# Kernel tuning notes

Hardware: AMD Instinct MI355X
Metric: run time of the kernel (lower is better)

## Reference

```python
import jax, jax.numpy as jnp
import numpy as np

BITS = 8
STEP = 2.0 ** (-5)
QMIN = -2.0 ** (BITS - 1)
QMAX = 2.0 ** (BITS - 1) - 1


def _q(x):
    # DFXP fixed-point fake-quantize: clamp(round(x/step), qmin, qmax)*step
    return jnp.clip(jnp.round(x / STEP), QMIN, QMAX) * STEP


@jax.custom_vjp
def fq(x):
    # ForwardQuantizer: quantize in fwd, straight-through grad
    return _q(x)

def _fq_fwd(x):
    return _q(x), None

def _fq_bwd(_, g):
    return (g,)

fq.defvjp(_fq_fwd, _fq_bwd)


def gq(x):
    # BackwardQuantizer: identity in forward (grad quantized only in bwd pass)
    return x


def setup_inputs() -> dict:
    key = jax.random.key(0)
    ks = jax.random.split(key, 5)
    B, I, H = 2048, 1024, 1024
    return {
        "X": jax.random.normal(ks[0], (B, I), dtype=jnp.float32),
        "h": jax.random.normal(ks[1], (B, H), dtype=jnp.float32),
        "c": jax.random.normal(ks[2], (B, H), dtype=jnp.float32),
        "weight": jax.random.normal(ks[3], (4 * H, I + H), dtype=jnp.float32) * (H ** -0.5),
        "bias": jax.random.normal(ks[4], (4 * H,), dtype=jnp.float32) * (H ** -0.5),
    }


def reference(X, h, c, weight, bias):
    # concat + input/weight/bias fake-quant
    Xh = fq(jnp.concatenate([X, h], axis=1))          # [B, I+H]
    Wq = fq(weight)                                    # [4H, I+H]
    bq = fq(bias)                                      # [4H]
    y = gq(Xh @ Wq.T + bq)                             # [B, 4H]
    i, f, g, o = jnp.split(y, 4, axis=1)
    i = fq(gq(jax.nn.sigmoid(i)))
    f = fq(gq(jax.nn.sigmoid(f)))
    g = fq(gq(jnp.tanh(g)))
    o = fq(gq(jax.nn.sigmoid(o)))
    cq = fq(c)
    c_new = gq(cq * f) + gq(i * g)
    cell_tanh = fq(gq(jnp.tanh(c_new)))
    h_new = gq(cell_tanh * o)
    return (h_new, c_new)
```

## Files before the change

### kernel.cpp

```cpp
#include <hip/hip_runtime.h>
#include <stdint.h>

#define B_DIM 2048
#define K_DIM 2048
#define N_PACK 4096

typedef int v4i __attribute__((ext_vector_type(4)));

__device__ __forceinline__ float fqf(float x) {
    float q = rintf(x * 32.0f);
    q = fminf(fmaxf(q, -128.0f), 127.0f);
    return q * 0.03125f;
}
__device__ __forceinline__ int q8i(float x) {
    float q = rintf(x * 32.0f);
    q = fminf(fmaxf(q, -128.0f), 127.0f);
    return (int)q;
}
__device__ __forceinline__ float fsigm(float x) {
    return __fdividef(1.0f, 1.0f + __expf(-x));
}
__device__ __forceinline__ float ftanh(float x) {
    return __fdividef(2.0f, 1.0f + __expf(-2.0f * x)) - 1.0f;
}

__global__ __launch_bounds__(256) void quant_pack(
    const float* __restrict__ X, const float* __restrict__ hI,
    const float* __restrict__ W, const float* __restrict__ bias,
    int8_t* __restrict__ Xhq, int8_t* __restrict__ Wq, float* __restrict__ bqp)
{
    const int bid = blockIdx.x;
    const int t = threadIdx.x;
    if (bid < 1024) {
        const int m = bid * 2 + (t >> 7);
        const int k0 = (t & 127) * 16;
        const float* src = (k0 < 1024) ? (X + (size_t)m * 1024 + k0)
                                       : (hI + (size_t)m * 1024 + (k0 - 1024));
        float4 v0 = *(const float4*)src;
        float4 v1 = *(const float4*)(src + 4);
        float4 v2 = *(const float4*)(src + 8);
        float4 v3 = *(const float4*)(src + 12);
        union { int8_t c[16]; v4i q; } u;
        u.c[0]  = (int8_t)q8i(v0.x); u.c[1]  = (int8_t)q8i(v0.y);
        u.c[2]  = (int8_t)q8i(v0.z); u.c[3]  = (int8_t)q8i(v0.w);
        u.c[4]  = (int8_t)q8i(v1.x); u.c[5]  = (int8_t)q8i(v1.y);
        u.c[6]  = (int8_t)q8i(v1.z); u.c[7]  = (int8_t)q8i(v1.w);
        u.c[8]  = (int8_t)q8i(v2.x); u.c[9]  = (int8_t)q8i(v2.y);
        u.c[10] = (int8_t)q8i(v2.z); u.c[11] = (int8_t)q8i(v2.w);
        u.c[12] = (int8_t)q8i(v3.x); u.c[13] = (int8_t)q8i(v3.y);
        u.c[14] = (int8_t)q8i(v3.z); u.c[15] = (int8_t)q8i(v3.w);
        *(v4i*)(Xhq + (size_t)m * K_DIM + k0) = u.q;
    } else if (bid < 3072) {
        const int r = (bid - 1024) * 2 + (t >> 7);
        const int gate = r >> 10, j = r & 1023;
        const int p = (j << 2) | gate;
        const int k0 = (t & 127) * 16;
        const float* src = W + (size_t)r * K_DIM + k0;
        float4 v0 = *(const float4*)src;
        float4 v1 = *(const float4*)(src + 4);
        float4 v2 = *(const float4*)(src + 8);
        float4 v3 = *(const float4*)(src + 12);
        union { int8_t c[16]; v4i q; } u;
        u.c[0]  = (int8_t)q8i(v0.x); u.c[1]  = (int8_t)q8i(v0.y);
        u.c[2]  = (int8_t)q8i(v0.z); u.c[3]  = (int8_t)q8i(v0.w);
        u.c[4]  = (int8_t)q8i(v1.x); u.c[5]  = (int8_t)q8i(v1.y);
        u.c[6]  = (int8_t)q8i(v1.z); u.c[7]  = (int8_t)q8i(v1.w);
        u.c[8]  = (int8_t)q8i(v2.x); u.c[9]  = (int8_t)q8i(v2.y);
        u.c[10] = (int8_t)q8i(v2.z); u.c[11] = (int8_t)q8i(v2.w);
        u.c[12] = (int8_t)q8i(v3.x); u.c[13] = (int8_t)q8i(v3.y);
        u.c[14] = (int8_t)q8i(v3.z); u.c[15] = (int8_t)q8i(v3.w);
        *(v4i*)(Wq + (size_t)p * K_DIM + k0) = u.q;
    } else {
        for (int idx = t; idx < N_PACK; idx += 256) {
            const int gate = idx >> 10, j = idx & 1023;
            bqp[(j << 2) | gate] = fqf(bias[idx]);
        }
    }
}

__global__ __launch_bounds__(512) void lstm_gemm(
    const int8_t* __restrict__ Xhq, const int8_t* __restrict__ Wq,
    const float* __restrict__ bqp, const float* __restrict__ cin,
    float* __restrict__ hout, float* __restrict__ cout_)
{
    __shared__ __align__(16) char raw[65536];
    const int t = threadIdx.x;
    const int l = t & 63;
    const int wave = t >> 6;
    const int wm = wave >> 2;
    const int wn = wave & 3;

    const int b = blockIdx.x;
    const int xcd = b & 7;
    const int slot = b >> 3;
    const int mt = ((xcd & 1) << 3) + (slot & 7);
    const int nt = ((xcd >> 1) << 3) + (slot >> 3);
    const int m0 = mt * 128;
    const int n0 = nt * 128;

    v4i acc[4][2];
    #pragma unroll
    for (int i = 0; i < 4; ++i)
        #pragma unroll
        for (int j = 0; j < 2; ++j)
            acc[i][j] = (v4i)0;

    const int srow = t >> 3;
    const int schunk = (t & 7) ^ (srow & 7);
    const int8_t* gA = Xhq + (size_t)(m0 + srow) * K_DIM + schunk * 16;
    const int8_t* gB = Wq  + (size_t)(n0 + srow) * K_DIM + schunk * 16;

    const int rrow = l & 15;
    const int lx = l & 7;

#define STAGE(p, kt) do { \
    char* Ad_ = raw + (p) * 32768; \
    char* Bd_ = raw + (p) * 32768 + 16384; \
    _Pragma("unroll") \
    for (int i_ = 0; i_ < 2; ++i_) { \
        __builtin_amdgcn_global_load_lds( \
            (const __attribute__((address_space(1))) uint32_t*)(gA + (size_t)(i_ * 64) * K_DIM + (kt) * 128), \
            (__attribute__((address_space(3))) uint32_t*)(Ad_ + i_ * 8192 + t * 16), 16, 0, 0); \
        __builtin_amdgcn_global_load_lds( \
            (const __attribute__((address_space(1))) uint32_t*)(gB + (size_t)(i_ * 64) * K_DIM + (kt) * 128), \
            (__attribute__((address_space(3))) uint32_t*)(Bd_ + i_ * 8192 + t * 16), 16, 0, 0); \
    } \
} while (0)

    STAGE(0, 0);

    for (int kt = 0; kt < 16; ++kt) {
        const int p = kt & 1;
        if (kt < 15) {
            STAGE(p ^ 1, kt + 1);
            asm volatile("s_waitcnt vmcnt(4)" ::: "memory");
        } else {
            asm volatile("s_waitcnt vmcnt(0)" ::: "memory");
        }
        asm volatile("s_barrier" ::: "memory");

        const char* As = raw + p * 32768;
        const char* Bs = raw + p * 32768 + 16384;
        v4i a[2][4], b2[2][2];
        #pragma unroll
        for (int kk = 0; kk < 2; ++kk) {
            const int c = kk * 4 + (l >> 4);
            const int sl = (c ^ lx) * 16;
            #pragma unroll
            for (int mf = 0; mf < 4; ++mf) {
                const int r = wm * 64 + mf * 16 + rrow;
                a[kk][mf] = *(const v4i*)(As + r * 128 + sl);
            }
            #pragma unroll
            for (int nf = 0; nf < 2; ++nf) {
                const int r = wn * 32 + nf * 16 + rrow;
                b2[kk][nf] = *(const v4i*)(Bs + r * 128 + sl);
            }
        }
        #pragma unroll
        for (int kk = 0; kk < 2; ++kk)
            #pragma unroll
            for (int mf = 0; mf < 4; ++mf)
                #pragma unroll
                for (int nf = 0; nf < 2; ++nf)
                    acc[mf][nf] = __builtin_amdgcn_mfma_i32_16x16x64_i8(a[kk][mf], b2[kk][nf], acc[mf][nf], 0, 0, 0);
        asm volatile("s_waitcnt lgkmcnt(0)" ::: "memory");
        asm volatile("s_barrier" ::: "memory");
    }

    float (*Cs)[132] = (float(*)[132])raw;
    const float sc = 0.0009765625f;
    for (int half = 0; half < 2; ++half) {
        __syncthreads();
        if (wm == half) {
            #pragma unroll
            for (int mf = 0; mf < 4; ++mf) {
                const int rb = mf * 16 + ((l >> 4) << 2);
                #pragma unroll
                for (int nf = 0; nf < 2; ++nf) {
                    const int col = wn * 32 + nf * 16 + (l & 15);
                    #pragma unroll
                    for (int rr = 0; rr < 4; ++rr)
                        Cs[rb + rr][col] = (float)acc[mf][nf][rr] * sc;
                }
            }
        }
        __syncthreads();
        #pragma unroll
        for (int it = 0; it < 4; ++it) {
            const int idx = it * 512 + t;
            const int row = idx >> 5;
            const int jl = idx & 31;
            float4 y = *(const float4*)&Cs[row][jl << 2];
            float4 bb = *(const float4*)&bqp[n0 + (jl << 2)];
            const int m = m0 + half * 64 + row;
            const int j = (n0 >> 2) + jl;
            const float ig = fqf(fsigm(y.x + bb.x));
            const float fg = fqf(fsigm(y.y + bb.y));
            const float gg = fqf(ftanh(y.z + bb.z));
            const float og = fqf(fsigm(y.w + bb.w));
            const float cq = fqf(cin[(size_t)m * 1024 + j]);
            const float cn = cq * fg + ig * gg;
            const float hn = fqf(ftanh(cn)) * og;
            hout[(size_t)m * 1024 + j] = hn;
            cout_[(size_t)m * 1024 + j] = cn;
        }
    }
}

extern "C" void kernel_launch(void* const* d_in, const int* in_sizes, int n_in,
                              void* d_out, int out_size, void* d_ws, size_t ws_size,
                              hipStream_t stream) {
    const float* X    = (const float*)d_in[0];
    const float* h    = (const float*)d_in[1];
    const float* c    = (const float*)d_in[2];
    const float* W    = (const float*)d_in[3];
    const float* bias = (const float*)d_in[4];

    float* out   = (float*)d_out;
    float* h_out = out;
    float* c_out = out + (size_t)B_DIM * 1024;

    char* ws = (char*)d_ws;
    int8_t* Xhq = (int8_t*)ws;
    int8_t* Wq  = (int8_t*)(ws + (size_t)4 * 1024 * 1024);
    float*  bqp = (float*)(ws + (size_t)12 * 1024 * 1024);

    quant_pack<<<3073, 256, 0, stream>>>(X, h, W, bias, Xhq, Wq, bqp);

    lstm_gemm<<<512, 512, 0, stream>>>(Xhq, Wq, bqp, c, h_out, c_out);
}
```

Measured before the change: 40.66 us.

## Pre-pack weights in MFMA fragment layout and load B directly to registers

The quant kernel now writes the int8 weights already arranged in per-16-row MFMA fragment order, transposing through LDS with fewer, larger blocks. The GEMM then loads B fragments straight from global memory into registers with double-buffered register sets, so only A is staged in LDS. This halves the GEMM's LDS footprint, which lets it request higher occupancy via launch bounds. The cost is more per-thread global load traffic for B, higher register pressure, and a more complex quant kernel with an LDS transpose and a barrier.

```diff
diff --git a/kernel.cpp b/kernel.cpp
--- a/kernel.cpp
+++ b/kernel.cpp
@@ -27,8 +27,9 @@
 __global__ __launch_bounds__(256) void quant_pack(
     const float* __restrict__ X, const float* __restrict__ hI,
     const float* __restrict__ W, const float* __restrict__ bias,
-    int8_t* __restrict__ Xhq, int8_t* __restrict__ Wq, float* __restrict__ bqp)
+    int8_t* __restrict__ Xhq, int8_t* __restrict__ Wq2, float* __restrict__ bqp)
 {
+    __shared__ __align__(16) char lds[16 * 2064];
     const int bid = blockIdx.x;
     const int t = threadIdx.x;
     if (bid < 1024) {
@@ -50,26 +51,28 @@
         u.c[12] = (int8_t)q8i(v3.x); u.c[13] = (int8_t)q8i(v3.y);
         u.c[14] = (int8_t)q8i(v3.z); u.c[15] = (int8_t)q8i(v3.w);
         *(v4i*)(Xhq + (size_t)m * K_DIM + k0) = u.q;
-    } else if (bid < 3072) {
-        const int r = (bid - 1024) * 2 + (t >> 7);
-        const int gate = r >> 10, j = r & 1023;
-        const int p = (j << 2) | gate;
-        const int k0 = (t & 127) * 16;
-        const float* src = W + (size_t)r * K_DIM + k0;
-        float4 v0 = *(const float4*)src;
-        float4 v1 = *(const float4*)(src + 4);
-        float4 v2 = *(const float4*)(src + 8);
-        float4 v3 = *(const float4*)(src + 12);
-        union { int8_t c[16]; v4i q; } u;
-        u.c[0]  = (int8_t)q8i(v0.x); u.c[1]  = (int8_t)q8i(v0.y);
-        u.c[2]  = (int8_t)q8i(v0.z); u.c[3]  = (int8_t)q8i(v0.w);
-        u.c[4]  = (int8_t)q8i(v1.x); u.c[5]  = (int8_t)q8i(v1.y);
-        u.c[6]  = (int8_t)q8i(v1.z); u.c[7]  = (int8_t)q8i(v1.w);
-        u.c[8]  = (int8_t)q8i(v2.x); u.c[9]  = (int8_t)q8i(v2.y);
-        u.c[10] = (int8_t)q8i(v2.z); u.c[11] = (int8_t)q8i(v2.w);
-        u.c[12] = (int8_t)q8i(v3.x); u.c[13] = (int8_t)q8i(v3.y);
-        u.c[14] = (int8_t)q8i(v3.z); u.c[15] = (int8_t)q8i(v3.w);
-        *(v4i*)(Wq + (size_t)p * K_DIM + k0) = u.q;
+    } else if (bid < 1280) {
+        const int c0 = bid - 1024;
+        for (int pi = 0; pi < 16; ++pi) {
+            const int r = (pi & 3) * 1024 + c0 * 4 + (pi >> 2);
+            const float* src = W + (size_t)r * K_DIM + t * 8;
+            float4 v0 = *(const float4*)src;
+            float4 v1 = *(const float4*)(src + 4);
+            union { int8_t c[8]; int64_t ll; } u;
+            u.c[0] = (int8_t)q8i(v0.x); u.c[1] = (int8_t)q8i(v0.y);
+            u.c[2] = (int8_t)q8i(v0.z); u.c[3] = (int8_t)q8i(v0.w);
+            u.c[4] = (int8_t)q8i(v1.x); u.c[5] = (int8_t)q8i(v1.y);
+            u.c[6] = (int8_t)q8i(v1.z); u.c[7] = (int8_t)q8i(v1.w);
+            *(int64_t*)(lds + pi * 2064 + t * 8) = u.ll;
+        }
+        __syncthreads();
+        const int w = t >> 6, l = t & 63;
+        #pragma unroll
+        for (int rd = 0; rd < 8; ++rd) {
+            const int c = rd * 4 + w;
+            v4i val = *(const v4i*)(lds + (l & 15) * 2064 + c * 64 + (l >> 4) * 16);
+            *(v4i*)(Wq2 + ((size_t)c0 << 15) + c * 1024 + l * 16) = val;
+        }
     } else {
         for (int idx = t; idx < N_PACK; idx += 256) {
             const int gate = idx >> 10, j = idx & 1023;
@@ -78,12 +81,12 @@
     }
 }
 
-__global__ __launch_bounds__(512) void lstm_gemm(
-    const int8_t* __restrict__ Xhq, const int8_t* __restrict__ Wq,
+__global__ __launch_bounds__(512, 4) void lstm_gemm(
+    const int8_t* __restrict__ Xhq, const int8_t* __restrict__ Wq2,
     const float* __restrict__ bqp, const float* __restrict__ cin,
     float* __restrict__ hout, float* __restrict__ cout_)
 {
-    __shared__ __align__(16) char raw[65536];
+    __shared__ __align__(16) char raw[33792];
     const int t = threadIdx.x;
     const int l = t & 63;
     const int wave = t >> 6;
@@ -108,65 +111,72 @@
     const int srow = t >> 3;
     const int schunk = (t & 7) ^ (srow & 7);
     const int8_t* gA = Xhq + (size_t)(m0 + srow) * K_DIM + schunk * 16;
-    const int8_t* gB = Wq  + (size_t)(n0 + srow) * K_DIM + schunk * 16;
-
-    const int rrow = l & 15;
-    const int lx = l & 7;
-
-#define STAGE(p, kt) do { \
-    char* Ad_ = raw + (p) * 32768; \
-    char* Bd_ = raw + (p) * 32768 + 16384; \
-    _Pragma("unroll") \
-    for (int i_ = 0; i_ < 2; ++i_) { \
+    const int8_t* gBf = Wq2 + (((size_t)(n0 >> 4) + wn * 2) << 15) + (size_t)l * 16;
+
+#define STAGE_A(p, kt) do { \
+    char* Ad_ = raw + (p) * 16384; \
+    _Pragma("unroll") \
+    for (int i_ = 0; i_ < 2; ++i_) \
         __builtin_amdgcn_global_load_lds( \
             (const __attribute__((address_space(1))) uint32_t*)(gA + (size_t)(i_ * 64) * K_DIM + (kt) * 128), \
             (__attribute__((address_space(3))) uint32_t*)(Ad_ + i_ * 8192 + t * 16), 16, 0, 0); \
-        __builtin_amdgcn_global_load_lds( \
-            (const __attribute__((address_space(1))) uint32_t*)(gB + (size_t)(i_ * 64) * K_DIM + (kt) * 128), \
-            (__attribute__((address_space(3))) uint32_t*)(Bd_ + i_ * 8192 + t * 16), 16, 0, 0); \
+} while (0)
+
+#define LOADB(dst, kt) do { \
+    _Pragma("unroll") \
+    for (int kk_ = 0; kk_ < 2; ++kk_) \
+        _Pragma("unroll") \
+        for (int nf_ = 0; nf_ < 2; ++nf_) \
+            dst[kk_][nf_] = *(const v4i*)(gBf + ((size_t)nf_ << 15) + (size_t)((kt) * 2 + kk_) * 1024); \
+} while (0)
+
+    v4i bA[2][2], bB[2][2];
+    STAGE_A(0, 0);
+    LOADB(bA, 0);
+
+    const int rrow = l & 15;
+    const int lx = l & 7;
+    const int g4 = l >> 4;
+
+#define ITER(kt, BU, BL) do { \
+    const int p_ = (kt) & 1; \
+    if ((kt) < 15) { \
+        STAGE_A(p_ ^ 1, (kt) + 1); \
+        LOADB(BL, (kt) + 1); \
+        asm volatile("s_waitcnt vmcnt(6)" ::: "memory"); \
+    } else { \
+        asm volatile("s_waitcnt vmcnt(0)" ::: "memory"); \
     } \
+    asm volatile("s_barrier" ::: "memory"); \
+    const char* As_ = raw + p_ * 16384; \
+    v4i a_[2][4]; \
+    _Pragma("unroll") \
+    for (int kk = 0; kk < 2; ++kk) { \
+        const int sl_ = ((kk * 4 + g4) ^ lx) * 16; \
+        _Pragma("unroll") \
+        for (int mf = 0; mf < 4; ++mf) \
+            a_[kk][mf] = *(const v4i*)(As_ + (wm * 64 + mf * 16 + rrow) * 128 + sl_); \
+    } \
+    _Pragma("unroll") \
+    for (int kk = 0; kk < 2; ++kk) \
+        _Pragma("unroll") \
+        for (int mf = 0; mf < 4; ++mf) \
+            _Pragma("unroll") \
+            for (int nf = 0; nf < 2; ++nf) \
+                acc[mf][nf] = __builtin_amdgcn_mfma_i32_16x16x64_i8( \
+                    a_[kk][mf], BU[kk][nf], acc[mf][nf], 0, 0, 0); \
+    asm volatile("s_waitcnt lgkmcnt(0)" ::: "memory"); \
+    asm volatile("s_barrier" ::: "memory"); \
 } while (0)
 
-    STAGE(0, 0);
-
-    for (int kt = 0; kt < 16; ++kt) {
-        const int p = kt & 1;
-        if (kt < 15) {
-            STAGE(p ^ 1, kt + 1);
-            asm volatile("s_waitcnt vmcnt(4)" ::: "memory");
-        } else {
-            asm volatile("s_waitcnt vmcnt(0)" ::: "memory");
-        }
-        asm volatile("s_barrier" ::: "memory");
-
-        const char* As = raw + p * 32768;
-        const char* Bs = raw + p * 32768 + 16384;
-        v4i a[2][4], b2[2][2];
-        #pragma unroll
-        for (int kk = 0; kk < 2; ++kk) {
-            const int c = kk * 4 + (l >> 4);
-            const int sl = (c ^ lx) * 16;
-            #pragma unroll
-            for (int mf = 0; mf < 4; ++mf) {
-                const int r = wm * 64 + mf * 16 + rrow;
-                a[kk][mf] = *(const v4i*)(As + r * 128 + sl);
-            }
-            #pragma unroll
-            for (int nf = 0; nf < 2; ++nf) {
-                const int r = wn * 32 + nf * 16 + rrow;
-                b2[kk][nf] = *(const v4i*)(Bs + r * 128 + sl);
-            }
-        }
-        #pragma unroll
-        for (int kk = 0; kk < 2; ++kk)
-            #pragma unroll
-            for (int mf = 0; mf < 4; ++mf)
-                #pragma unroll
-                for (int nf = 0; nf < 2; ++nf)
-                    acc[mf][nf] = __builtin_amdgcn_mfma_i32_16x16x64_i8(a[kk][mf], b2[kk][nf], acc[mf][nf], 0, 0, 0);
-        asm volatile("s_waitcnt lgkmcnt(0)" ::: "memory");
-        asm volatile("s_barrier" ::: "memory");
+    for (int k2 = 0; k2 < 8; ++k2) {
+        ITER(2 * k2,     bA, bB);
+        ITER(2 * k2 + 1, bB, bA);
     }
+
+#undef STAGE_A
+#undef LOADB
+#undef ITER
 
     float (*Cs)[132] = (float(*)[132])raw;
     const float sc = 0.0009765625f;
@@ -223,10 +233,10 @@
 
     char* ws = (char*)d_ws;
     int8_t* Xhq = (int8_t*)ws;
-    int8_t* Wq  = (int8_t*)(ws + (size_t)4 * 1024 * 1024);
+    int8_t* Wq2 = (int8_t*)(ws + (size_t)4 * 1024 * 1024);
     float*  bqp = (float*)(ws + (size_t)12 * 1024 * 1024);
 
-    quant_pack<<<3073, 256, 0, stream>>>(X, h, W, bias, Xhq, Wq, bqp);
-
-    lstm_gemm<<<512, 512, 0, stream>>>(Xhq, Wq, bqp, c, h_out, c_out);
-}
+    quant_pack<<<1281, 256, 0, stream>>>(X, h, W, bias, Xhq, Wq2, bqp);
+
+    lstm_gemm<<<512, 512, 0, stream>>>(Xhq, Wq2, bqp, c, h_out, c_out);
+}
```

Measured after the change: 43.81 us. 7.8% more time.
